# Kernel optimization log

Hardware: AMD Instinct MI355X
Metric: run time of the kernel (lower is better)

## Reference

```python
import jax, jax.numpy as jnp
import numpy as np

D_MODEL = 2048
N_HEADS = 16
N_KV = 4
D_HEAD = D_MODEL // N_HEADS  # 128
N_REP = N_HEADS // N_KV      # 4
ROPE_BASE = 1000000.0


def _rope_tables(T, d_head, dtype):
    # inv_freq = (1/base)^(2i/d) for i in [0, d/2)
    i = jnp.arange(d_head // 2, dtype=jnp.float32)
    inv_freq = (1.0 / ROPE_BASE) ** (2.0 * i / d_head)
    theta = jnp.arange(T, dtype=jnp.float32)[:, None] * inv_freq[None, :]  # [T, d/2]
    theta = jnp.concatenate([theta, theta], axis=-1)                        # [T, d]
    return jnp.sin(theta).astype(dtype), jnp.cos(theta).astype(dtype)


def _apply_rope(x, sin, cos):
    # x: [B, h, T, d]; sin/cos: [T, d]
    x1, x2 = jnp.split(x, 2, axis=-1)
    rot = jnp.concatenate([-x2, x1], axis=-1)
    return cos[None, None] * x + sin[None, None] * rot


def setup_inputs() -> dict:
    key = jax.random.key(0)
    ks = jax.random.split(key, 9)
    B, T = 2, 2048
    s_in = 1.0 / np.sqrt(D_MODEL)
    return {
        "x": jax.random.normal(ks[0], (B, T, D_MODEL), jnp.float32),
        "wq": jax.random.normal(ks[1], (D_MODEL, N_HEADS * D_HEAD), jnp.float32) * s_in,
        "bq": jax.random.normal(ks[2], (N_HEADS * D_HEAD,), jnp.float32) * 0.02,
        "wk": jax.random.normal(ks[3], (D_MODEL, N_KV * D_HEAD), jnp.float32) * s_in,
        "bk": jax.random.normal(ks[4], (N_KV * D_HEAD,), jnp.float32) * 0.02,
        "wv": jax.random.normal(ks[5], (D_MODEL, N_KV * D_HEAD), jnp.float32) * s_in,
        "bv": jax.random.normal(ks[6], (N_KV * D_HEAD,), jnp.float32) * 0.02,
        "wo": jax.random.normal(ks[7], (D_MODEL, D_MODEL), jnp.float32) * s_in,
    }


def reference(x, wq, bq, wk, bk, wv, bv, wo):
    B, T, C = x.shape
    sin, cos = _rope_tables(T, D_HEAD, x.dtype)

    q = (x @ wq + bq).reshape(B, T, N_HEADS, D_HEAD).transpose(0, 2, 1, 3)  # [B,H,T,d]
    k = (x @ wk + bk).reshape(B, T, N_KV, D_HEAD).transpose(0, 2, 1, 3)     # [B,KV,T,d]
    v = (x @ wv + bv).reshape(B, T, N_KV, D_HEAD).transpose(0, 2, 1, 3)     # [B,KV,T,d]

    q = _apply_rope(q, sin, cos)
    k = _apply_rope(k, sin, cos)

    # GQA: group query heads as [B, KV, rep, T, d] to broadcast against k/v
    qg = q.reshape(B, N_KV, N_REP, T, D_HEAD)
    scale = 1.0 / jnp.sqrt(jnp.asarray(D_HEAD, x.dtype))
    scores = jnp.einsum('bkrqd,bksd->bkrqs', qg, k) * scale  # [B,KV,rep,T,S]

    causal = jnp.tril(jnp.ones((T, T), dtype=bool))
    neg = jnp.asarray(jnp.finfo(x.dtype).min, x.dtype)
    scores = jnp.where(causal[None, None, None], scores, neg)
    p = jax.nn.softmax(scores, axis=-1)

    out = jnp.einsum('bkrqs,bksd->bkrqd', p, v)               # [B,KV,rep,T,d]
    out = out.reshape(B, N_HEADS, T, D_HEAD).transpose(0, 2, 1, 3).reshape(B, T, C)
    return out @ wo, k, v
```

## Files before the change

kernel.cpp:

```cpp
#include <hip/hip_runtime.h>
#include <hip/hip_bf16.h>
#include <math.h>

#define BB 2
#define TT 2048
#define DMODEL 2048
#define NH 16
#define NKV 4
#define DH 128
#define NQKV 3072
#define MM (BB*TT)

typedef unsigned short u16;
typedef unsigned int u32;

typedef __bf16 bf16x8 __attribute__((ext_vector_type(8)));
typedef __bf16 bf16x4 __attribute__((ext_vector_type(4)));
typedef short short4v __attribute__((ext_vector_type(4)));
typedef float f32x4 __attribute__((ext_vector_type(4)));

__device__ __forceinline__ u16 f2b(float f) {
  union { float f; u32 u; } v; v.f = f;
  u32 r = v.u + 0x7fffu + ((v.u >> 16) & 1u);
  return (u16)(r >> 16);
}
__device__ __forceinline__ float b2f(u16 h) {
  union { u32 u; float f; } v; v.u = ((u32)h) << 16;
  return v.f;
}
__device__ __forceinline__ u32 pack2bf(float x, float y) {
  union { float f; u32 u; } a, b; a.f = x; b.f = y;
  return ((a.u + 0x8000u) >> 16) | ((b.u + 0x8000u) & 0xffff0000u);
}

__device__ __forceinline__ void gload16(const void* g, void* l) {
  __builtin_amdgcn_global_load_lds(
      (const __attribute__((address_space(1))) unsigned int*)g,
      (__attribute__((address_space(3))) unsigned int*)l, 16, 0, 0);
}

__device__ __forceinline__ float fast_exp2(float x) {
#if __has_builtin(__builtin_amdgcn_exp2f)
  return __builtin_amdgcn_exp2f(x);
#else
  return __expf(x * 0.6931471805599453f);
#endif
}

__device__ __forceinline__ f32x4 mfma16(bf16x4 a, bf16x4 b, f32x4 c) {
#if __has_builtin(__builtin_amdgcn_mfma_f32_16x16x16bf16_1k)
  union { bf16x4 b; short4v s; } ua, ub;
  ua.b = a; ub.b = b;
  return __builtin_amdgcn_mfma_f32_16x16x16bf16_1k(ua.s, ub.s, c, 0, 0, 0);
#elif __has_builtin(__builtin_amdgcn_mfma_f32_16x16x16_bf16)
  return __builtin_amdgcn_mfma_f32_16x16x16_bf16(a, b, c, 0, 0, 0);
#else
  asm volatile("v_mfma_f32_16x16x16_bf16 %0, %1, %2, %0"
               : "+v"(c) : "v"(a), "v"(b));
  return c;
#endif
}

__global__ void cvt_x_kernel(const float* __restrict__ x, u16* __restrict__ xb, int n4) {
  int i = blockIdx.x * 256 + threadIdx.x;
  if (i < n4) {
    float4 v = ((const float4*)x)[i];
    u32 lo = (u32)f2b(v.x) | ((u32)f2b(v.y) << 16);
    u32 hi = (u32)f2b(v.z) | ((u32)f2b(v.w) << 16);
    uint2 r; r.x = lo; r.y = hi;
    ((uint2*)xb)[i] = r;
  }
}

__global__ void rope_table_kernel(float2* __restrict__ tab) {
  int i = blockIdx.x * 256 + threadIdx.x;
  int t = i >> 6, d = i & 63;
  float inv = exp2f(-(float)d * 0.31143075889569023f);
  float th = (float)t * inv;
  float2 cs; cs.x = cosf(th); cs.y = sinf(th);
  tab[i] = cs;
}

__global__ void transpose_cvt_all_kernel(const float* __restrict__ wq,
                                         const float* __restrict__ wk,
                                         const float* __restrict__ wv,
                                         const float* __restrict__ wo,
                                         u16* __restrict__ wqkvT,
                                         u16* __restrict__ woT) {
  __shared__ u16 t[64][65];
  int bx = blockIdx.x;
  const float* src; u16* dst; int srcCols, rowOff, cb;
  if (bx < 32)      { src = wq; dst = wqkvT; srcCols = 2048; rowOff = 0;    cb = bx; }
  else if (bx < 40) { src = wk; dst = wqkvT; srcCols = 512;  rowOff = 2048; cb = bx - 32; }
  else if (bx < 48) { src = wv; dst = wqkvT; srcCols = 512;  rowOff = 2560; cb = bx - 40; }
  else              { src = wo; dst = woT;   srcCols = 2048; rowOff = 0;    cb = bx - 48; }
  int c0 = cb * 64, r0 = blockIdx.y * 64;
  int tid = threadIdx.x;
  for (int i = tid; i < 4096; i += 256) {
    int r = i >> 6, c = i & 63;
    t[r][c] = f2b(src[(size_t)(r0 + r) * srcCols + c0 + c]);
  }
  __syncthreads();
  for (int i = tid; i < 4096; i += 256) {
    int n = i >> 6, k = i & 63;
    dst[(size_t)(rowOff + c0 + n) * 2048 + r0 + k] = t[k][n];
  }
}


#define BARRIER asm volatile("s_barrier" ::: "memory")

#define STAGE_A(H, KT, RB) do { \
    const u16* g_ = gA + (size_t)(H) * 262144 + (size_t)(KT) * 64; \
    gload16(g_,          sm + (RB) + tid * 8); \
    gload16(g_ + 131072, sm + (RB) + 4096 + tid * 8); \
  } while (0)

#define STAGE_B(H, KT, RB) do { \
    const u16* g_ = gB + (size_t)(H) * 262144 + (size_t)(KT) * 64; \
    gload16(g_,          sm + (RB) + tid * 8); \
    gload16(g_ + 131072, sm + (RB) + 4096 + tid * 8); \
  } while (0)

#define LDA2(DST, BU, MH) do { \
    const u16* ab_ = sm + (BU) + (MH) * 8192 + lra * 64; \
    _Pragma("unroll") \
    for (int mi = 0; mi < 4; mi++) { \
      DST[mi][0] = *(const bf16x8*)&ab_[mi * 1024 + as0]; \
      DST[mi][1] = *(const bf16x8*)&ab_[mi * 1024 + as1]; \
    } \
  } while (0)

#define LDB2(DST, BU, NL) do { \
    const u16* bb_ = sm + (BU) + 16384 + hb * 8192 + lrb * 64; \
    _Pragma("unroll") \
    for (int nj = 0; nj < 2; nj++) { \
      DST[nj][0] = *(const bf16x8*)&bb_[((NL)*2+nj) * 1024 + bs0]; \
      DST[nj][1] = *(const bf16x8*)&bb_[((NL)*2+nj) * 1024 + bs1]; \
    } \
  } while (0)

#define MFMAQ2(AR, BR, MH, NL) do { \
    _Pragma("unroll") \
    for (int mi = 0; mi < 4; mi++) \
      _Pragma("unroll") \
      for (int nj = 0; nj < 2; nj++) { \
        acc[(MH)*4+mi][(NL)*2+nj] = __builtin_amdgcn_mfma_f32_16x16x32_bf16( \
            AR[mi][0], BR[nj][0], acc[(MH)*4+mi][(NL)*2+nj], 0, 0, 0); \
        acc[(MH)*4+mi][(NL)*2+nj] = __builtin_amdgcn_mfma_f32_16x16x32_bf16( \
            AR[mi][1], BR[nj][1], acc[(MH)*4+mi][(NL)*2+nj], 0, 0, 0); \
      } \
  } while (0)

#define TILE4P(BU, OBU, KA1, KN) do { \
     \
    LDB2(b23, BU, 1); \
    STAGE_A(1, KA1, (OBU) + 8192); \
    BARRIER; \
    __builtin_amdgcn_s_setprio(1); MFMAQ2(aA, b01, 0, 0); __builtin_amdgcn_s_setprio(0); \
    BARRIER; \
     \
     \
    LDA2(aB, BU, 1); \
    STAGE_A(0, KN, (BU)); \
    BARRIER; \
    __builtin_amdgcn_s_setprio(1); MFMAQ2(aA, b23, 0, 1); __builtin_amdgcn_s_setprio(0); \
    asm volatile("s_waitcnt vmcnt(4)\n\ts_barrier" ::: "memory"); \
     \
    LDA2(aA, OBU, 0); \
    STAGE_B(0, KN, (BU) + 16384); \
    BARRIER; \
    __builtin_amdgcn_s_setprio(1); MFMAQ2(aB, b01, 1, 0); __builtin_amdgcn_s_setprio(0); \
    BARRIER; \
     \
     \
    LDB2(b01, OBU, 0); \
    STAGE_B(1, KN, (BU) + 24576); \
    BARRIER; \
    __builtin_amdgcn_s_setprio(1); MFMAQ2(aB, b23, 1, 1); __builtin_amdgcn_s_setprio(0); \
    asm volatile("s_waitcnt vmcnt(6)\n\ts_barrier" ::: "memory"); \
  } while (0)

__global__ __launch_bounds__(512, 2) void gemm_qkv_kernel(
    const u16* __restrict__ A, const u16* __restrict__ Bt,
    const float* __restrict__ bq, const float* __restrict__ bk,
    const float* __restrict__ bv, const float2* __restrict__ rtab,
    u16* __restrict__ qb, u16* __restrict__ kb, u16* __restrict__ vt,
    float* __restrict__ outK, float* __restrict__ outV) {
  __shared__ __align__(16) u16 sm[65536];
  const int tid  = threadIdx.x;
  const int lane = tid & 63;
  const int wave = tid >> 6;
  const int wm   = wave >> 2;
  const int wn   = wave & 3;
  const int quad = lane >> 4;
  const int l16  = lane & 15;
  const int m0 = blockIdx.y * 256;
  const int n0 = blockIdx.x * 256;
  const int bx = blockIdx.x;

  const int srow = tid >> 3;
  const int sch  = (tid & 7) ^ (srow & 7);
  const u16* gA = A  + (size_t)(m0 + srow) * 2048 + sch * 8;
  const u16* gB = Bt + (size_t)(n0 + srow) * 2048 + sch * 8;

  const int lra = wm * 64 + l16;
  const int lrb = (wn & 1) * 64 + l16;
  const int hb  = wn >> 1;
  const int as0 = ((quad)     ^ (lra & 7)) << 3;
  const int as1 = ((quad + 4) ^ (lra & 7)) << 3;
  const int bs0 = ((quad)     ^ (lrb & 7)) << 3;
  const int bs1 = ((quad + 4) ^ (lrb & 7)) << 3;

  bf16x8 aA[4][2], aB[4][2], b01[2][2], b23[2][2];
  f32x4 acc[8][4];
  const f32x4 zero = {0.f, 0.f, 0.f, 0.f};
#pragma unroll
  for (int i = 0; i < 8; i++)
#pragma unroll
    for (int j = 0; j < 4; j++) acc[i][j] = zero;

  STAGE_A(0, 0, 0);
  STAGE_B(0, 0, 16384);
  STAGE_B(1, 0, 24576);
  STAGE_A(1, 0, 8192);
  STAGE_A(0, 1, 32768);
  STAGE_B(0, 1, 32768 + 16384);
  STAGE_B(1, 1, 32768 + 24576);
  asm volatile("s_waitcnt vmcnt(6)\n\ts_barrier" ::: "memory");

  LDA2(aA, 0, 0);
  LDB2(b01, 0, 0);

#pragma unroll 1
  for (int it2 = 0; it2 < 16; ++it2) {
    const int ka1 = (2 * it2 + 1) & 31;
    const int kn0 = (2 * it2 + 2) & 31;
    const int kn1 = (2 * it2 + 3) & 31;
    TILE4P(0,     32768, ka1, kn0);
    TILE4P(32768, 0,     kn0, kn1);
  }

  asm volatile("s_waitcnt vmcnt(0)\n\ts_barrier" ::: "memory");

  const int cls = (bx < 8) ? 0 : ((bx < 10) ? 1 : 2);
#pragma unroll
  for (int nf = 0; nf < 4; nf++) {
    int col = wn * 64 + nf * 16 + l16;
    int gcol = n0 + col;
    float bval = (cls == 0) ? bq[gcol] : ((cls == 1) ? bk[gcol - 2048] : bv[gcol - 2560]);
#pragma unroll
    for (int mh = 0; mh < 2; mh++)
#pragma unroll
      for (int mi = 0; mi < 4; mi++)
#pragma unroll
        for (int r = 0; r < 4; r++) {
          int row = mh * 128 + wm * 64 + mi * 16 + quad * 4 + r;
          int ci = (row * 256 + col) ^ ((row & 7) << 3);
          sm[ci] = f2b(acc[mh * 4 + mi][nf][r] + bval);
        }
  }
  __syncthreads();

  const int bidx = m0 >> 11;
  const int trow0 = m0 & 2047;

  if (cls < 2) {
    const int isQ = (cls == 0);
#pragma unroll
    for (int itq = 0; itq < 8; itq++) {
      int id = tid + itq * 512;
      int lh = id >> 11;
      int rem = id & 2047;
      int row = rem >> 3, oc = rem & 7;
      int t = trow0 + row;
      int rl = t & 63, ttile = t >> 6;
      int sw = (row & 7) << 3;
      int i0 = (row * 256 + lh * 128 + oc * 8);
      uint4 lo = *(const uint4*)&sm[i0 ^ sw];
      uint4 hi = *(const uint4*)&sm[(i0 + 64) ^ sw];
      const u16* plo = (const u16*)&lo;
      const u16* phi = (const u16*)&hi;
      u16 y1[8], y2[8];
      float f1[8], f2v[8];
#pragma unroll
      for (int j = 0; j < 8; j++) {
        float2 cs = rtab[(t << 6) + oc * 8 + j];
        float x1 = b2f(plo[j]), x2 = b2f(phi[j]);
        f1[j]  = cs.x * x1 - cs.y * x2;
        f2v[j] = cs.x * x2 + cs.y * x1;
        y1[j] = f2b(f1[j]);
        y2[j] = f2b(f2v[j]);
      }
      if (isQ) {
        int hh = bx * 2 + lh;
        size_t tb = ((size_t)(bidx * NH + hh) * 32 + ttile) * 8192;
        *(uint4*)&qb[tb + (size_t)((oc)     * 64 + rl) * 8] = *(const uint4*)y1;
        *(uint4*)&qb[tb + (size_t)((oc + 8) * 64 + rl) * 8] = *(const uint4*)y2;
      } else {
        int hh = bx * 2 + lh - 16;
        size_t tb = ((size_t)(bidx * NKV + hh) * 32 + ttile) * 8192;
        *(uint4*)&kb[tb + (size_t)((oc)     * 64 + rl) * 8] = *(const uint4*)y1;
        *(uint4*)&kb[tb + (size_t)((oc + 8) * 64 + rl) * 8] = *(const uint4*)y2;
        size_t base = ((size_t)(bidx * NKV + hh) * TT + t) * DH + oc * 8;
        *(float4*)&outK[base]          = *(const float4*)&f1[0];
        *(float4*)&outK[base + 4]      = *(const float4*)&f1[4];
        *(float4*)&outK[base + 64]     = *(const float4*)&f2v[0];
        *(float4*)&outK[base + 64 + 4] = *(const float4*)&f2v[4];
      }
    }
  } else {
#pragma unroll
    for (int itv = 0; itv < 16; itv++) {
      int id = tid + itv * 512;
      int lh = id >> 12;
      int rem = id & 4095;
      int row = rem >> 4, oc = rem & 15;
      int kvh = bx * 2 + lh - 20;
      int i0 = (row * 256 + lh * 128 + oc * 8) ^ ((row & 7) << 3);
      uint4 v = *(const uint4*)&sm[i0];
      const u16* pv = (const u16*)&v;
      float f[8];
#pragma unroll
      for (int j = 0; j < 8; j++) f[j] = b2f(pv[j]);
      size_t base = ((size_t)(bidx * NKV + kvh) * TT + trow0 + row) * DH + oc * 8;
      *(float4*)&outV[base]     = *(const float4*)&f[0];
      *(float4*)&outV[base + 4] = *(const float4*)&f[4];
    }
#pragma unroll
    for (int itv = 0; itv < 16; itv++) {
      int id = tid + itv * 512;
      int lh = id >> 12;
      int rem = id & 4095;
      int st = rem >> 10;
      int rem2 = rem & 1023;
      int chunk = rem2 >> 7, dl = rem2 & 127;
      int m = chunk >> 2, qd = chunk & 3;
      int kvh = bx * 2 + lh - 20;
      u16 tmp[8];
#pragma unroll
      for (int e = 0; e < 8; e++) {
        int srw = (2 * m + (e >> 2)) * 16 + qd * 4 + (e & 3);
        int row = st * 64 + srw;
        int idx = (row * 256 + lh * 128 + dl) ^ ((row & 7) << 3);
        tmp[e] = sm[idx];
      }
      int tt = (trow0 >> 6) + st;
      size_t tilebase = ((size_t)(bidx * NKV + kvh) * 32 + tt) * 8192;
      *(uint4*)&vt[tilebase + (size_t)(chunk * 128 + dl) * 8] = *(const uint4*)tmp;
    }
  }
}

__global__ __launch_bounds__(256, 3) void gemm_out_kernel(
    const u16* __restrict__ A, const u16* __restrict__ Bt,
    float* __restrict__ Cout, int M, int N, int K) {
  __shared__ __align__(16) u16 smo[16384];
  const int tid  = threadIdx.x;
  const int lane = tid & 63;
  const int wave = tid >> 6;
  const int quad = lane >> 4;
  const int l16  = lane & 15;
  const int m0 = blockIdx.y * 128;
  const int n0 = blockIdx.x * 128;
  const int wrow = (wave >> 1) * 64;
  const int wcol = (wave & 1) * 64;

  f32x4 acc[4][4];
  const f32x4 zero = {0.f, 0.f, 0.f, 0.f};
#pragma unroll
  for (int i = 0; i < 4; i++)
#pragma unroll
    for (int j = 0; j < 4; j++) acc[i][j] = zero;

  const int srow = tid >> 2;
  const int scol = (tid & 3) * 8;
  const u16* ga = A  + (size_t)(m0 + srow) * K + scol;
  const u16* gb = Bt + (size_t)(n0 + srow) * K + scol;

  gload16(ga,                  &smo[tid * 8]);
  gload16(ga + (size_t)64 * K, &smo[2048 + tid * 8]);
  gload16(gb,                  &smo[4096 + tid * 8]);
  gload16(gb + (size_t)64 * K, &smo[6144 + tid * 8]);

  for (int k0 = 0; k0 < K; k0 += 32) {
    const int p = (k0 >> 5) & 1;
    const int kn = (k0 + 32 == K) ? 0 : k0 + 32;
    u16* nb = &smo[(p ^ 1) * 8192];
    gload16(ga + kn,                  nb + tid * 8);
    gload16(ga + kn + (size_t)64 * K, nb + 2048 + tid * 8);
    gload16(gb + kn,                  nb + 4096 + tid * 8);
    gload16(gb + kn + (size_t)64 * K, nb + 6144 + tid * 8);
    asm volatile("s_waitcnt vmcnt(4)\n\ts_barrier" ::: "memory");
    const u16* cb = &smo[p * 8192];
    bf16x8 af[4], bf[4];
#pragma unroll
    for (int mi = 0; mi < 4; mi++)
      af[mi] = *(const bf16x8*)&cb[(wrow + mi * 16 + l16) * 32 + quad * 8];
#pragma unroll
    for (int ni = 0; ni < 4; ni++)
      bf[ni] = *(const bf16x8*)&cb[4096 + (wcol + ni * 16 + l16) * 32 + quad * 8];
    asm volatile("s_waitcnt lgkmcnt(0)\n\ts_barrier" ::: "memory");
#pragma unroll
    for (int mi = 0; mi < 4; mi++)
#pragma unroll
      for (int ni = 0; ni < 4; ni++)
        acc[mi][ni] = __builtin_amdgcn_mfma_f32_16x16x32_bf16(af[mi], bf[ni], acc[mi][ni], 0, 0, 0);
  }
  asm volatile("s_waitcnt vmcnt(0)" ::: "memory");

#pragma unroll
  for (int ni = 0; ni < 4; ni++) {
    int gcol = n0 + wcol + ni * 16 + l16;
#pragma unroll
    for (int mi = 0; mi < 4; mi++) {
#pragma unroll
      for (int r = 0; r < 4; r++) {
        int grow = m0 + wrow + mi * 16 + quad * 4 + r;
        Cout[(size_t)grow * N + gcol] = acc[mi][ni][r];
      }
    }
  }
}

__global__ __launch_bounds__(256, 2) void attn_kernel(
    const u16* __restrict__ Qt, const u16* __restrict__ Kt,
    const u16* __restrict__ Vt, u16* __restrict__ Ob) {
  __shared__ __align__(16) u16 sm[24576];
  u16* vbuf = sm + 16384;

  const int bh = blockIdx.y;
  const int b = bh >> 4, h = bh & 15, kv = h >> 2;
  const int tid = threadIdx.x;
  const int lane = tid & 63;
  const int wave = tid >> 6;
  const int quad = lane >> 4;
  const int l16 = lane & 15;

  const u16* qbase = Qt + (size_t)(b * NH + h) * 32 * 8192;
  const u16* kbase = Kt + (size_t)(b * NKV + kv) * 32 * 8192;
  const u16* vbase = Vt + (size_t)(b * NKV + kv) * 32 * 8192;

  const f32x4 zero = {0.f, 0.f, 0.f, 0.f};
  const float SC2 = 0.08838834764831845f * 1.4426950408889634f;
  const float NEGINF = -__builtin_inff();

  int par = 0;

#pragma unroll
  for (int pp = 0; pp < 4; pp++)
    gload16(kbase + pp * 2048 + tid * 8, sm + pp * 2048 + tid * 8);

  for (int half = 0; half < 2; ++half) {
    const int qt = half ? (31 - (int)blockIdx.x) : (int)blockIdx.x;
    const int q0 = qt * 64;
    const u16* qtile = qbase + (size_t)qt * 8192;
    const int qrel = wave * 16 + l16;

    bf16x8 qf[4];
#pragma unroll
    for (int kc = 0; kc < 4; kc++)
      qf[kc] = *(const bf16x8*)&qtile[(size_t)((kc * 4 + quad) * 64 + qrel) * 8];

    float mrow = NEGINF, lrow = 0.f;
    f32x4 o[8];
#pragma unroll
    for (int d = 0; d < 8; d++) o[d] = zero;

    for (int kt = 0; kt <= qt; ++kt) {
      u16* kb_c = sm + par * 8192;
      u16* kb_n = sm + (par ^ 1) * 8192;
      const int ktn = (kt < qt) ? kt + 1 : 0;
      const u16* vsrc = vbase + (size_t)kt * 8192;
      const u16* knxt = kbase + (size_t)ktn * 8192;
#pragma unroll
      for (int pp = 0; pp < 4; pp++)
        gload16(vsrc + pp * 2048 + tid * 8, vbuf + pp * 2048 + tid * 8);
#pragma unroll
      for (int pp = 0; pp < 4; pp++)
        gload16(knxt + pp * 2048 + tid * 8, kb_n + pp * 2048 + tid * 8);
      asm volatile("s_waitcnt vmcnt(8)\n\ts_barrier" ::: "memory");

      f32x4 sv[4];
#pragma unroll
      for (int mt = 0; mt < 4; mt++) sv[mt] = zero;
      __builtin_amdgcn_s_setprio(1);
#pragma unroll
      for (int kc = 0; kc < 4; kc++) {
#pragma unroll
        for (int mt = 0; mt < 4; mt++) {
          bf16x8 kf = *(const bf16x8*)&kb_c[(size_t)((kc * 4 + quad) * 64 + mt * 16 + l16) * 8];
          sv[mt] = __builtin_amdgcn_mfma_f32_16x16x32_bf16(kf, qf[kc], sv[mt], 0, 0, 0);
        }
      }
      __builtin_amdgcn_s_setprio(0);

      if (kt == qt) {
#pragma unroll
        for (int mt = 0; mt < 4; mt++)
#pragma unroll
          for (int r = 0; r < 4; r++) {
            int srel = mt * 16 + quad * 4 + r;
            if (srel > qrel) sv[mt][r] = NEGINF;
          }
      }
      float mraw = NEGINF;
#pragma unroll
      for (int mt = 0; mt < 4; mt++)
#pragma unroll
        for (int r = 0; r < 4; r++) mraw = fmaxf(mraw, sv[mt][r]);
      mraw = fmaxf(mraw, __shfl_xor(mraw, 16));
      mraw = fmaxf(mraw, __shfl_xor(mraw, 32));

      bool noresc = __all(mraw <= mrow + 8.0f);
      float mnew = noresc ? mrow : fmaxf(mrow, mraw);
      float msc = mnew * SC2;
      float lsum = 0.f;
#pragma unroll
      for (int mt = 0; mt < 4; mt++) {
#pragma unroll
        for (int r = 0; r < 4; r++) {
          float pe = fast_exp2(__builtin_fmaf(sv[mt][r], SC2, -msc));
          sv[mt][r] = pe;
          lsum += pe;
        }
      }
      if (noresc) {
        lrow += lsum;
      } else {
        float alpha = fast_exp2((mrow - mnew) * SC2);
        mrow = mnew;
        lrow = lrow * alpha + lsum;
#pragma unroll
        for (int dt = 0; dt < 8; dt++) {
          o[dt][0] *= alpha; o[dt][1] *= alpha; o[dt][2] *= alpha; o[dt][3] *= alpha;
        }
      }
      bf16x4 pb[4];
#pragma unroll
      for (int mt = 0; mt < 4; mt++) {
        union { u32 u[2]; bf16x4 v; } pu;
        pu.u[0] = pack2bf(sv[mt][0], sv[mt][1]);
        pu.u[1] = pack2bf(sv[mt][2], sv[mt][3]);
        pb[mt] = pu.v;
      }

      asm volatile("s_waitcnt vmcnt(4)\n\ts_barrier" ::: "memory");
      __builtin_amdgcn_s_setprio(1);
#pragma unroll
      for (int m = 0; m < 2; m++) {
#pragma unroll
        for (int dt = 0; dt < 8; dt++) {
          bf16x8 vf = *(const bf16x8*)&vbuf[(size_t)(((m * 4 + quad) * 128) + dt * 16 + l16) * 8];
          bf16x4 vlo = __builtin_shufflevector(vf, vf, 0, 1, 2, 3);
          bf16x4 vhi = __builtin_shufflevector(vf, vf, 4, 5, 6, 7);
          o[dt] = mfma16(vlo, pb[2 * m],     o[dt]);
          o[dt] = mfma16(vhi, pb[2 * m + 1], o[dt]);
        }
      }
      __builtin_amdgcn_s_setprio(0);
      asm volatile("s_barrier" ::: "memory");
      par ^= 1;
    }

    lrow += __shfl_xor(lrow, 16);
    lrow += __shfl_xor(lrow, 32);
    float inv = 1.0f / lrow;
    int t = q0 + qrel;
    size_t rowbase = (size_t)(b * TT + t) * DMODEL + h * DH;
#pragma unroll
    for (int dt = 0; dt < 8; dt++) {
      uint2 w;
      w.x = pack2bf(o[dt][0] * inv, o[dt][1] * inv);
      w.y = pack2bf(o[dt][2] * inv, o[dt][3] * inv);
      *(uint2*)&Ob[rowbase + dt * 16 + quad * 4] = w;
    }
  }
  asm volatile("s_waitcnt vmcnt(0)" ::: "memory");
}

extern "C" void kernel_launch(void* const* d_in, const int* in_sizes, int n_in,
                              void* d_out, int out_size, void* d_ws, size_t ws_size,
                              hipStream_t stream) {
  (void)in_sizes; (void)n_in; (void)out_size; (void)ws_size;
  const float* x  = (const float*)d_in[0];
  const float* wq = (const float*)d_in[1];
  const float* bq = (const float*)d_in[2];
  const float* wk = (const float*)d_in[3];
  const float* bk = (const float*)d_in[4];
  const float* wv = (const float*)d_in[5];
  const float* bv = (const float*)d_in[6];
  const float* wo = (const float*)d_in[7];
  float* out = (float*)d_out;

  char* ws = (char*)d_ws;
  u16*    xb    = (u16*)(ws);
  u16*    wqkvT = (u16*)(ws + 16777216);
  u16*    woT   = (u16*)(ws + 29360128);
  float2* rtab  = (float2*)(ws + 37748736);
  u16*    qb    = (u16*)(ws + 38797312);
  u16*    kb    = (u16*)(ws + 55574528);
  u16*    vt    = (u16*)(ws + 59768832);
  u16*    ob    = (u16*)(ws + 63963136);

  float* outK = out + (size_t)BB * TT * DMODEL;
  float* outV = outK + (size_t)BB * NKV * TT * DH;

  cvt_x_kernel<<<8192, 256, 0, stream>>>(x, xb, (BB * TT * DMODEL) / 4);
  rope_table_kernel<<<512, 256, 0, stream>>>(rtab);
  transpose_cvt_all_kernel<<<dim3(80, 32), 256, 0, stream>>>(wq, wk, wv, wo, wqkvT, woT);

  gemm_qkv_kernel<<<dim3(NQKV / 256, MM / 256), 512, 0, stream>>>(
      xb, wqkvT, bq, bk, bv, rtab, qb, kb, vt, outK, outV);

  attn_kernel<<<dim3(16, BB * NH), 256, 0, stream>>>(qb, kb, vt, ob);

  gemm_out_kernel<<<dim3(DMODEL / 128, MM / 128), 256, 0, stream>>>(
      ob, woT, out, MM, DMODEL, DMODEL);
}
```

Measured before the change: 301.2 us.

## Merge prep kernels into one launch and read V directly from global in attention

After: 313.8 us. +4.2%, slower.

```diff
diff --git a/kernel.cpp b/kernel.cpp
--- a/kernel.cpp
+++ b/kernel.cpp
@@ -61,49 +61,46 @@
 #endif
 }
 
-__global__ void cvt_x_kernel(const float* __restrict__ x, u16* __restrict__ xb, int n4) {
-  int i = blockIdx.x * 256 + threadIdx.x;
-  if (i < n4) {
+__global__ void prep_kernel(const float* __restrict__ x, u16* __restrict__ xb,
+                            float2* __restrict__ rtab,
+                            const float* __restrict__ wq, const float* __restrict__ wk,
+                            const float* __restrict__ wv, const float* __restrict__ wo,
+                            u16* __restrict__ wqkvT, u16* __restrict__ woT) {
+  __shared__ u16 t[64][65];
+  const int bx = blockIdx.x;
+  const int tid = threadIdx.x;
+  if (bx < 8192) {
+    int i = bx * 256 + tid;
     float4 v = ((const float4*)x)[i];
     u32 lo = (u32)f2b(v.x) | ((u32)f2b(v.y) << 16);
     u32 hi = (u32)f2b(v.z) | ((u32)f2b(v.w) << 16);
     uint2 r; r.x = lo; r.y = hi;
     ((uint2*)xb)[i] = r;
-  }
-}
-
-__global__ void rope_table_kernel(float2* __restrict__ tab) {
-  int i = blockIdx.x * 256 + threadIdx.x;
-  int t = i >> 6, d = i & 63;
-  float inv = exp2f(-(float)d * 0.31143075889569023f);
-  float th = (float)t * inv;
-  float2 cs; cs.x = cosf(th); cs.y = sinf(th);
-  tab[i] = cs;
-}
-
-__global__ void transpose_cvt_all_kernel(const float* __restrict__ wq,
-                                         const float* __restrict__ wk,
-                                         const float* __restrict__ wv,
-                                         const float* __restrict__ wo,
-                                         u16* __restrict__ wqkvT,
-                                         u16* __restrict__ woT) {
-  __shared__ u16 t[64][65];
-  int bx = blockIdx.x;
-  const float* src; u16* dst; int srcCols, rowOff, cb;
-  if (bx < 32)      { src = wq; dst = wqkvT; srcCols = 2048; rowOff = 0;    cb = bx; }
-  else if (bx < 40) { src = wk; dst = wqkvT; srcCols = 512;  rowOff = 2048; cb = bx - 32; }
-  else if (bx < 48) { src = wv; dst = wqkvT; srcCols = 512;  rowOff = 2560; cb = bx - 40; }
-  else              { src = wo; dst = woT;   srcCols = 2048; rowOff = 0;    cb = bx - 48; }
-  int c0 = cb * 64, r0 = blockIdx.y * 64;
-  int tid = threadIdx.x;
-  for (int i = tid; i < 4096; i += 256) {
-    int r = i >> 6, c = i & 63;
-    t[r][c] = f2b(src[(size_t)(r0 + r) * srcCols + c0 + c]);
-  }
-  __syncthreads();
-  for (int i = tid; i < 4096; i += 256) {
-    int n = i >> 6, k = i & 63;
-    dst[(size_t)(rowOff + c0 + n) * 2048 + r0 + k] = t[k][n];
+  } else if (bx < 8704) {
+    int i = (bx - 8192) * 256 + tid;
+    int tt = i >> 6, d = i & 63;
+    float inv = exp2f(-(float)d * 0.31143075889569023f);
+    float th = (float)tt * inv;
+    float2 cs; cs.x = cosf(th); cs.y = sinf(th);
+    rtab[i] = cs;
+  } else {
+    int tb = bx - 8704;
+    int tx = tb % 80, ty = tb / 80;
+    const float* src; u16* dst; int srcCols, rowOff, cb;
+    if (tx < 32)      { src = wq; dst = wqkvT; srcCols = 2048; rowOff = 0;    cb = tx; }
+    else if (tx < 40) { src = wk; dst = wqkvT; srcCols = 512;  rowOff = 2048; cb = tx - 32; }
+    else if (tx < 48) { src = wv; dst = wqkvT; srcCols = 512;  rowOff = 2560; cb = tx - 40; }
+    else              { src = wo; dst = woT;   srcCols = 2048; rowOff = 0;    cb = tx - 48; }
+    int c0 = cb * 64, r0 = ty * 64;
+    for (int i = tid; i < 4096; i += 256) {
+      int r = i >> 6, c = i & 63;
+      t[r][c] = f2b(src[(size_t)(r0 + r) * srcCols + c0 + c]);
+    }
+    __syncthreads();
+    for (int i = tid; i < 4096; i += 256) {
+      int n = i >> 6, k = i & 63;
+      dst[(size_t)(rowOff + c0 + n) * 2048 + r0 + k] = t[k][n];
+    }
   }
 }
 
@@ -153,27 +150,21 @@
   } while (0)
 
 #define TILE4P(BU, OBU, KA1, KN) do { \
-     \
     LDB2(b23, BU, 1); \
     STAGE_A(1, KA1, (OBU) + 8192); \
     BARRIER; \
     __builtin_amdgcn_s_setprio(1); MFMAQ2(aA, b01, 0, 0); __builtin_amdgcn_s_setprio(0); \
     BARRIER; \
-     \
-     \
     LDA2(aB, BU, 1); \
     STAGE_A(0, KN, (BU)); \
     BARRIER; \
     __builtin_amdgcn_s_setprio(1); MFMAQ2(aA, b23, 0, 1); __builtin_amdgcn_s_setprio(0); \
     asm volatile("s_waitcnt vmcnt(4)\n\ts_barrier" ::: "memory"); \
-     \
     LDA2(aA, OBU, 0); \
     STAGE_B(0, KN, (BU) + 16384); \
     BARRIER; \
     __builtin_amdgcn_s_setprio(1); MFMAQ2(aB, b01, 1, 0); __builtin_amdgcn_s_setprio(0); \
     BARRIER; \
-     \
-     \
     LDB2(b01, OBU, 0); \
     STAGE_B(1, KN, (BU) + 24576); \
     BARRIER; \
@@ -426,8 +417,7 @@
 __global__ __launch_bounds__(256, 2) void attn_kernel(
     const u16* __restrict__ Qt, const u16* __restrict__ Kt,
     const u16* __restrict__ Vt, u16* __restrict__ Ob) {
-  __shared__ __align__(16) u16 sm[24576];
-  u16* vbuf = sm + 16384;
+  __shared__ __align__(16) u16 sm[16384];
 
   const int bh = blockIdx.y;
   const int b = bh >> 4, h = bh & 15, kv = h >> 2;
@@ -475,11 +465,8 @@
       const u16* knxt = kbase + (size_t)ktn * 8192;
 #pragma unroll
       for (int pp = 0; pp < 4; pp++)
-        gload16(vsrc + pp * 2048 + tid * 8, vbuf + pp * 2048 + tid * 8);
-#pragma unroll
-      for (int pp = 0; pp < 4; pp++)
         gload16(knxt + pp * 2048 + tid * 8, kb_n + pp * 2048 + tid * 8);
-      asm volatile("s_waitcnt vmcnt(8)\n\ts_barrier" ::: "memory");
+      asm volatile("s_waitcnt vmcnt(4)\n\ts_barrier" ::: "memory");
 
       f32x4 sv[4];
 #pragma unroll
@@ -545,13 +532,12 @@
         pb[mt] = pu.v;
       }
 
-      asm volatile("s_waitcnt vmcnt(4)\n\ts_barrier" ::: "memory");
       __builtin_amdgcn_s_setprio(1);
 #pragma unroll
       for (int m = 0; m < 2; m++) {
 #pragma unroll
         for (int dt = 0; dt < 8; dt++) {
-          bf16x8 vf = *(const bf16x8*)&vbuf[(size_t)(((m * 4 + quad) * 128) + dt * 16 + l16) * 8];
+          bf16x8 vf = *(const bf16x8*)&vsrc[(size_t)(((m * 4 + quad) * 128) + dt * 16 + l16) * 8];
           bf16x4 vlo = __builtin_shufflevector(vf, vf, 0, 1, 2, 3);
           bf16x4 vhi = __builtin_shufflevector(vf, vf, 4, 5, 6, 7);
           o[dt] = mfma16(vlo, pb[2 * m],     o[dt]);
@@ -606,9 +592,7 @@
   float* outK = out + (size_t)BB * TT * DMODEL;
   float* outV = outK + (size_t)BB * NKV * TT * DH;
 
-  cvt_x_kernel<<<8192, 256, 0, stream>>>(x, xb, (BB * TT * DMODEL) / 4);
-  rope_table_kernel<<<512, 256, 0, stream>>>(rtab);
-  transpose_cvt_all_kernel<<<dim3(80, 32), 256, 0, stream>>>(wq, wk, wv, wo, wqkvT, woT);
+  prep_kernel<<<11264, 256, 0, stream>>>(x, xb, rtab, wq, wk, wv, wo, wqkvT, woT);
 
   gemm_qkv_kernel<<<dim3(NQKV / 256, MM / 256), 512, 0, stream>>>(
       xb, wqkvT, bq, bk, bv, rtab, qb, kb, vt, outK, outV);
```
